# Kernel optimization log

Measured on AMD Instinct MI355X. Metric: run time of the kernel, lower is better.

Reference implementation:

```python
import jax, jax.numpy as jnp
import numpy as np

B, D, H, W = 64, 256, 32, 32
K, DC = 1024, 128  # codebook size, codebook dim = D // 2
BETA = 0.25


def setup_inputs() -> dict:
    key = jax.random.key(0)
    ks = jax.random.split(key, 4)
    return {
        "x": jax.random.normal(ks[0], (B, D, H, W), dtype=jnp.float32),
        "pre_W": jax.random.normal(ks[1], (DC, D), dtype=jnp.float32) * (1.0 / np.sqrt(D)),
        "pre_b": jnp.zeros((DC,), dtype=jnp.float32),
        "post_W": jax.random.normal(ks[2], (D, DC), dtype=jnp.float32) * (1.0 / np.sqrt(DC)),
        "post_b": jnp.zeros((D,), dtype=jnp.float32),
        "lookup_table": jax.random.normal(ks[3], (K, DC), dtype=jnp.float32) * (1.0 / np.sqrt(DC)),
    }


def reference(x, pre_W, pre_b, post_W, post_b, lookup_table):
    sg = jax.lax.stop_gradient
    b, d, h, w = x.shape
    # pre-quant 1x1 conv: [b, d, h, w] -> [b, dc, h, w]
    z = jnp.einsum("bchw,oc->bohw", x, pre_W) + pre_b[None, :, None, None]
    # flatten tokens: [b*h*w, dc]
    zf = z.transpose(0, 2, 3, 1).reshape(-1, DC)
    # squared distances to codebook (argmin identical to cdist argmin)
    d2 = (
        jnp.sum(zf * zf, axis=1, keepdims=True)
        - 2.0 * zf @ lookup_table.T
        + jnp.sum(lookup_table * lookup_table, axis=1)[None, :]
    )  # [N, K]
    q = jnp.argmin(d2, axis=1)  # [N]
    x_e = lookup_table[q].reshape(b, h, w, DC).transpose(0, 3, 1, 2)  # [b, dc, h, w]
    # losses (enable_ema_update = False path)
    codebook_loss = jnp.mean((sg(z) - x_e) ** 2)
    commitment_loss = BETA * jnp.mean((z - sg(x_e)) ** 2)
    loss = (1.0 - BETA) * codebook_loss + commitment_loss
    # straight-through estimator
    z_st = z + sg(x_e - z)
    # post-quant 1x1 conv: [b, dc, h, w] -> [b, d, h, w]
    out = jnp.einsum("bchw,oc->bohw", z_st, post_W) + post_b[None, :, None, None]
    # perplexity from empirical code usage
    counts = jnp.zeros((K,), dtype=jnp.float32).at[q].add(1.0)
    e_mean = counts / q.shape[0]
    perplexity = jnp.exp(-jnp.sum(e_mean * jnp.log(e_mean + 1e-10)))
    q_map = q.reshape(b, h, w)
    return out, loss, q_map, perplexity
```

## Files before the change

kernel.cpp:

```cpp
#include <hip/hip_runtime.h>
#include <cstdint>

#define NB   64
#define ND   256
#define NHW  1024
#define NTOK 65536
#define NDC  128
#define NK   1024

#define OFF_LOSS 16777216
#define OFF_Q    16777217
#define OFF_PERP 16842753

#define GAPTHR 1e-3f
#define NEGINF (-3.402823466e38f)

typedef short short8 __attribute__((ext_vector_type(8)));
typedef float f32x4 __attribute__((ext_vector_type(4)));

__device__ __forceinline__ unsigned short f2bf(float f) {
  unsigned u = __float_as_uint(f);
  u += 0x7FFFu + ((u >> 16) & 1u);
  return (unsigned short)(u >> 16);
}
__device__ __forceinline__ float bf2f(unsigned short h) {
  return __uint_as_float(((unsigned)h) << 16);
}

__device__ __forceinline__ void gll16(const void* g, void* l) {
  __builtin_amdgcn_global_load_lds(
      (const __attribute__((address_space(1))) unsigned int*)g,
      (__attribute__((address_space(3))) unsigned int*)l, 16, 0, 0);
}

__global__ __launch_bounds__(256) void k_init(
    const float* __restrict__ lut, const float* __restrict__ preW,
    const float* __restrict__ postW,
    unsigned short* __restrict__ ch,
    unsigned short* __restrict__ pwh, unsigned short* __restrict__ pwl,
    unsigned short* __restrict__ qwh, unsigned short* __restrict__ qwl,
    float* __restrict__ nhn, double* __restrict__ cn2d,
    int* __restrict__ counts, double* __restrict__ lossAcc, int* __restrict__ ctr) {
  int tid = blockIdx.x * 256 + threadIdx.x;
  int stride = gridDim.x * 256;
  for (int i = tid; i < NK * NDC; i += stride) {
    int code = i >> 7, c = i & 127;
    float f = lut[i];
    unsigned short h1 = f2bf(f);
    float r = f - bf2f(h1);
    ch[code * 256 + c] = h1;
    ch[code * 256 + 128 + c] = f2bf(r);
  }
  for (int i = tid; i < NDC * ND; i += stride) {
    float f = preW[i];
    unsigned u = __float_as_uint(f);
    float lf = f - __uint_as_float(u & 0xffff0000u);
    pwh[i] = (unsigned short)(u >> 16);
    pwl[i] = (unsigned short)(__float_as_uint(lf) >> 16);
  }
  for (int i = tid; i < ND * NDC; i += stride) {
    float f = postW[i];
    unsigned u = __float_as_uint(f);
    float lf = f - __uint_as_float(u & 0xffff0000u);
    qwh[i] = (unsigned short)(u >> 16);
    qwl[i] = (unsigned short)(__float_as_uint(lf) >> 16);
  }
  if (tid < NK) {
    float s = 0.f;
    double sd = 0.0;
    for (int c = 0; c < NDC; c++) {
      float v = lut[tid * NDC + c];
      s = fmaf(v, v, s);
      sd = fma((double)v, (double)v, sd);
    }
    nhn[tid] = -0.5f * s;
    cn2d[tid] = sd;
    counts[tid] = 0;
  }
  if (tid == 0) { *lossAcc = 0.0; *ctr = 0; }
}

__global__ __launch_bounds__(256, 1) void k_preconv(
    const float* __restrict__ x, const unsigned short* __restrict__ pwh,
    const unsigned short* __restrict__ pwl, const float* __restrict__ pre_b,
    float* __restrict__ zf) {
  __shared__ __align__(16) float xs[2][32 * 256];
  int bx = blockIdx.x;
  int b = bx >> 2, p0 = (bx & 3) * 256;
  int tid = threadIdx.x;
  int lane = tid & 63, w = tid >> 6;
  int g = lane >> 4, l15 = lane & 15;
  const char* xb = (const char*)(x + (size_t)b * (ND * NHW) + p0);

  #pragma unroll
  for (int i = 0; i < 8; ++i) {
    int o = i * 4096 + tid * 16;
    int chl = o >> 10;
    int col = (o & 1023) ^ (((chl >> 3) & 3) << 5);
    gll16(xb + (size_t)chl * 4096 + col, ((char*)&xs[0][0]) + o);
  }
  asm volatile("s_waitcnt vmcnt(0)" ::: "memory");
  __syncthreads();

  f32x4 acc[8][4];
  #pragma unroll
  for (int rt = 0; rt < 8; ++rt)
    #pragma unroll
    for (int ct = 0; ct < 4; ++ct) acc[rt][ct] = (f32x4){0.f, 0.f, 0.f, 0.f};

  int cur = 0;
  for (int ks = 0; ks < 8; ++ks) {
    if (ks < 7) {
      const char* gb = xb + (size_t)(ks + 1) * 32 * 4096;
      #pragma unroll
      for (int i = 0; i < 8; ++i) {
        int o = i * 4096 + tid * 16;
        int chl = o >> 10;
        int col = (o & 1023) ^ (((chl >> 3) & 3) << 5);
        gll16(gb + (size_t)chl * 4096 + col, ((char*)&xs[cur ^ 1][0]) + o);
      }
    }
    int k0 = ks * 32;
    short8 bh[4], bl[4];
    #pragma unroll
    for (int ct = 0; ct < 4; ++ct) {
      int tok = w * 64 + ct * 16 + l15;
      int tswz = tok ^ (g << 3);
      #pragma unroll
      for (int j = 0; j < 8; ++j) {
        float f = xs[cur][(g * 8 + j) * 256 + tswz];
        unsigned u = __float_as_uint(f);
        float lf = f - __uint_as_float(u & 0xffff0000u);
        bh[ct][j] = (short)(u >> 16);
        bl[ct][j] = (short)(__float_as_uint(lf) >> 16);
      }
    }
    #pragma unroll
    for (int rt = 0; rt < 8; ++rt) {
      short8 ah = *reinterpret_cast<const short8*>(&pwh[(rt * 16 + l15) * ND + k0 + g * 8]);
      short8 al = *reinterpret_cast<const short8*>(&pwl[(rt * 16 + l15) * ND + k0 + g * 8]);
      #pragma unroll
      for (int ct = 0; ct < 4; ++ct) {
        acc[rt][ct] = __builtin_amdgcn_mfma_f32_16x16x32_bf16(ah, bh[ct], acc[rt][ct], 0, 0, 0);
        acc[rt][ct] = __builtin_amdgcn_mfma_f32_16x16x32_bf16(ah, bl[ct], acc[rt][ct], 0, 0, 0);
        acc[rt][ct] = __builtin_amdgcn_mfma_f32_16x16x32_bf16(al, bh[ct], acc[rt][ct], 0, 0, 0);
      }
    }
    asm volatile("s_waitcnt vmcnt(0)" ::: "memory");
    __syncthreads();
    cur ^= 1;
  }

  #pragma unroll
  for (int rt = 0; rt < 8; ++rt) {
    float4 bb = *reinterpret_cast<const float4*>(&pre_b[rt * 16 + g * 4]);
    #pragma unroll
    for (int ct = 0; ct < 4; ++ct) {
      int n = bx * 256 + w * 64 + ct * 16 + l15;
      float4 v;
      v.x = acc[rt][ct][0] + bb.x;
      v.y = acc[rt][ct][1] + bb.y;
      v.z = acc[rt][ct][2] + bb.z;
      v.w = acc[rt][ct][3] + bb.w;
      *reinterpret_cast<float4*>(&zf[(size_t)n * NDC + rt * 16 + g * 4]) = v;
    }
  }
}

__global__ __launch_bounds__(256, 2) void k_dist(
    const float* __restrict__ zf, const unsigned short* __restrict__ ch,
    const float* __restrict__ nhn,
    int* __restrict__ q, int* __restrict__ list, int* __restrict__ ctr,
    double* __restrict__ lossAcc) {
  __shared__ __align__(16) short chbuf[2][8192];
  __shared__ float HnLds[NK];
  __shared__ float zn2Lds[4][2][16];
  __shared__ float red[256];
  int tid = threadIdx.x;
  int lane = tid & 63, w = tid >> 6;
  int g = lane >> 4;
  int n0 = blockIdx.x * 128;

  for (int i = tid; i < NK; i += 256) HnLds[i] = nhn[i];

  short8 az[2][8];
  {
    int arow = lane & 15;
    #pragma unroll
    for (int rt = 0; rt < 2; ++rt) {
      const float* zr = zf + (size_t)(n0 + w * 32 + rt * 16 + arow) * NDC;
      float sq = 0.f;
      #pragma unroll
      for (int f = 0; f < 4; ++f) {
        const float* p = zr + f * 32 + g * 8;
        float4 v0 = *reinterpret_cast<const float4*>(p);
        float4 v1 = *reinterpret_cast<const float4*>(p + 4);
        float vv[8] = {v0.x, v0.y, v0.z, v0.w, v1.x, v1.y, v1.z, v1.w};
        short8 hi, lo;
        #pragma unroll
        for (int j = 0; j < 8; ++j) {
          sq = fmaf(vv[j], vv[j], sq);
          unsigned short h1 = f2bf(vv[j]);
          float r = vv[j] - bf2f(h1);
          hi[j] = (short)h1;
          lo[j] = (short)f2bf(r);
        }
        az[rt][f] = hi;
        az[rt][4 + f] = lo;
      }
      sq += __shfl_xor(sq, 16, 64);
      sq += __shfl_xor(sq, 32, 64);
      if (g == 0) zn2Lds[w][rt][arow] = sq;
    }
  }

  float best[2][4], sec[2][4];
  int bidx[2][4];
  #pragma unroll
  for (int rt = 0; rt < 2; ++rt)
    #pragma unroll
    for (int r = 0; r < 4; ++r) { best[rt][r] = NEGINF; sec[rt][r] = NEGINF; bidx[rt][r] = 0; }

  const char* chg = (const char*)ch;
  {
    const char* gb = chg + 0;
    #pragma unroll
    for (int rr = 0; rr < 4; ++rr) {
      int o = rr * 4096 + tid * 16;
      int so = o ^ (((o >> 9) & 7) << 4);
      gll16(gb + so, ((char*)&chbuf[0][0]) + o);
    }
  }
  asm volatile("s_waitcnt vmcnt(0)" ::: "memory");
  __syncthreads();

  int cur = 0;
  for (int chunk = 0; chunk < 32; ++chunk) {
    if (chunk < 31) {
      const char* gb = chg + (chunk + 1) * 16384;
      #pragma unroll
      for (int rr = 0; rr < 4; ++rr) {
        int o = rr * 4096 + tid * 16;
        int so = o ^ (((o >> 9) & 7) << 4);
        gll16(gb + so, ((char*)&chbuf[cur ^ 1][0]) + o);
      }
    }
    const char* cb = (const char*)&chbuf[cur][0];
    for (int ct = 0; ct < 2; ++ct) {
      int codeg = chunk * 32 + ct * 16 + (lane & 15);
      float nh = HnLds[codeg];
      short8 bc[8];
      #pragma unroll
      for (int f = 0; f < 8; ++f) {
        int byte = ((lane & 15) + ct * 16) * 512 + f * 64 + g * 16;
        byte ^= ((lane & 7) << 4);
        bc[f] = *reinterpret_cast<const short8*>(cb + byte);
      }
      f32x4 acc0 = {nh, nh, nh, nh};
      f32x4 acc1 = {nh, nh, nh, nh};
      #pragma unroll
      for (int j = 0; j < 4; ++j) {
        acc0 = __builtin_amdgcn_mfma_f32_16x16x32_bf16(az[0][j], bc[j], acc0, 0, 0, 0);
        acc1 = __builtin_amdgcn_mfma_f32_16x16x32_bf16(az[1][j], bc[j], acc1, 0, 0, 0);
        acc0 = __builtin_amdgcn_mfma_f32_16x16x32_bf16(az[0][j], bc[4 + j], acc0, 0, 0, 0);
        acc1 = __builtin_amdgcn_mfma_f32_16x16x32_bf16(az[1][j], bc[4 + j], acc1, 0, 0, 0);
        acc0 = __builtin_amdgcn_mfma_f32_16x16x32_bf16(az[0][4 + j], bc[j], acc0, 0, 0, 0);
        acc1 = __builtin_amdgcn_mfma_f32_16x16x32_bf16(az[1][4 + j], bc[j], acc1, 0, 0, 0);
      }
      #pragma unroll
      for (int r = 0; r < 4; ++r) {
        float s0 = acc0[r];
        bool t0 = s0 > best[0][r];
        bidx[0][r] = t0 ? codeg : bidx[0][r];
        sec[0][r] = fmaxf(sec[0][r], fminf(s0, best[0][r]));
        best[0][r] = fmaxf(s0, best[0][r]);
        float s1 = acc1[r];
        bool t1 = s1 > best[1][r];
        bidx[1][r] = t1 ? codeg : bidx[1][r];
        sec[1][r] = fmaxf(sec[1][r], fminf(s1, best[1][r]));
        best[1][r] = fmaxf(s1, best[1][r]);
      }
    }
    asm volatile("s_waitcnt vmcnt(0)" ::: "memory");
    __syncthreads();
    cur ^= 1;
  }

  float lsum = 0.f;
  #pragma unroll
  for (int rt = 0; rt < 2; ++rt) {
    #pragma unroll
    for (int r = 0; r < 4; ++r) {
      float b = best[rt][r];
      float s2 = sec[rt][r];
      int bi_ = bidx[rt][r];
      #pragma unroll
      for (int m = 1; m < 16; m <<= 1) {
        float ob = __shfl_xor(b, m, 64);
        float os = __shfl_xor(s2, m, 64);
        int oi = __shfl_xor(bi_, m, 64);
        float ns = fmaxf(fmaxf(s2, os), fminf(b, ob));
        bool take = (ob > b) || (ob == b && oi < bi_);
        b = take ? ob : b;
        bi_ = take ? oi : bi_;
        s2 = ns;
      }
      if ((lane & 15) == 0) {
        int token = n0 + w * 32 + rt * 16 + g * 4 + r;
        q[token] = bi_;
        if (b - s2 < GAPTHR) {
          int pos = atomicAdd(ctr, 1);
          list[pos] = token;
        }
        lsum += zn2Lds[w][rt][g * 4 + r] - 2.0f * b;
      }
    }
  }
  red[tid] = lsum;
  __syncthreads();
  for (int s = 128; s > 0; s >>= 1) {
    if (tid < s) red[tid] += red[tid + s];
    __syncthreads();
  }
  if (tid == 0) atomicAdd(lossAcc, (double)red[0]);
}

__global__ __launch_bounds__(256) void k_rescore(
    const float* __restrict__ x, const float* __restrict__ preW,
    const float* __restrict__ pre_b, const float* __restrict__ lut,
    const double* __restrict__ cn2d,
    const int* __restrict__ list, const int* __restrict__ ctr, int* __restrict__ q) {
  __shared__ float xs[4][256];
  __shared__ double zs[4][128];
  __shared__ double rd[4][256];
  __shared__ int    rc[4][256];
  int nf = *ctr;
  int tid = threadIdx.x;
  int w = tid >> 6, lane = tid & 63;
  for (int g0 = blockIdx.x * 4; g0 < nf; g0 += gridDim.x * 4) {
    int nt = nf - g0; if (nt > 4) nt = 4;
    #pragma unroll
    for (int t = 0; t < 4; ++t) {
      int token = list[g0 + (t < nt ? t : 0)];
      int b = token >> 10, p = token & 1023;
      xs[t][tid] = x[(size_t)(b * ND + tid) * NHW + p];
    }
    __syncthreads();
    #pragma unroll
    for (int rep = 0; rep < 2; ++rep) {
      int idx = rep * 256 + tid;
      int t = idx >> 7, dc = idx & 127;
      double acc = (double)pre_b[dc];
      const float* wr = preW + (size_t)dc * ND;
      #pragma unroll 4
      for (int d = 0; d < ND; d += 4) {
        float4 wv = *reinterpret_cast<const float4*>(wr + d);
        acc = fma((double)wv.x, (double)xs[t][d + 0], acc);
        acc = fma((double)wv.y, (double)xs[t][d + 1], acc);
        acc = fma((double)wv.z, (double)xs[t][d + 2], acc);
        acc = fma((double)wv.w, (double)xs[t][d + 3], acc);
      }
      zs[t][dc] = acc;
    }
    __syncthreads();
    double bd[4]; int bc_[4];
    #pragma unroll
    for (int t = 0; t < 4; ++t) { bd[t] = 1e300; bc_[t] = 0x7fffffff; }
    for (int cc = 0; cc < 4; ++cc) {
      int c = cc * 256 + tid;
      const float* cr = lut + (size_t)c * NDC;
      double a0 = 0.0, a1 = 0.0, a2 = 0.0, a3 = 0.0;
      #pragma unroll 4
      for (int k = 0; k < NDC; ++k) {
        double lc = (double)cr[k];
        a0 = fma(zs[0][k], lc, a0);
        a1 = fma(zs[1][k], lc, a1);
        a2 = fma(zs[2][k], lc, a2);
        a3 = fma(zs[3][k], lc, a3);
      }
      double cn = cn2d[c];
      double d0 = cn - 2.0 * a0; if (d0 < bd[0]) { bd[0] = d0; bc_[0] = c; }
      double d1 = cn - 2.0 * a1; if (d1 < bd[1]) { bd[1] = d1; bc_[1] = c; }
      double d2 = cn - 2.0 * a2; if (d2 < bd[2]) { bd[2] = d2; bc_[2] = c; }
      double d3 = cn - 2.0 * a3; if (d3 < bd[3]) { bd[3] = d3; bc_[3] = c; }
    }
    #pragma unroll
    for (int t = 0; t < 4; ++t) { rd[t][tid] = bd[t]; rc[t][tid] = bc_[t]; }
    __syncthreads();
    {
      double b_ = rd[w][lane]; int c_ = rc[w][lane];
      #pragma unroll
      for (int s = 64; s < 256; s += 64) {
        double ob = rd[w][lane + s]; int oc = rc[w][lane + s];
        if (ob < b_ || (ob == b_ && oc < c_)) { b_ = ob; c_ = oc; }
      }
      #pragma unroll
      for (int m = 1; m < 64; m <<= 1) {
        double ob = __shfl_xor(b_, m, 64);
        int oc = __shfl_xor(c_, m, 64);
        if (ob < b_ || (ob == b_ && oc < c_)) { b_ = ob; c_ = oc; }
      }
      if (lane == 0 && w < nt) q[list[g0 + w]] = c_;
    }
    __syncthreads();
  }
}

__global__ __launch_bounds__(256, 3) void k_post(
    const float* __restrict__ lut,
    const int* __restrict__ q, const unsigned short* __restrict__ qwh,
    const unsigned short* __restrict__ qwl, const float* __restrict__ post_b,
    float* __restrict__ out,
    int* __restrict__ counts, float* __restrict__ outq) {
  int bx = blockIdx.x;
  int n0 = (bx >> 1) * 128;
  int oh = (bx & 1) * 128;
  int b = n0 >> 10, p0 = n0 & 1023;
  int tid = threadIdx.x;
  int lane = tid & 63, w = tid >> 6;
  int g = lane >> 4, l15 = lane & 15;

  int qv[2];
  #pragma unroll
  for (int ct = 0; ct < 2; ++ct) qv[ct] = q[n0 + w * 32 + ct * 16 + l15];

  float4 ga[2][4][2];
  #pragma unroll
  for (int ct = 0; ct < 2; ++ct) {
    const float* xr0 = lut + (size_t)qv[ct] * NDC + g * 8;
    #pragma unroll
    for (int ks = 0; ks < 4; ++ks) {
      ga[ct][ks][0] = *reinterpret_cast<const float4*>(xr0 + ks * 32);
      ga[ct][ks][1] = *reinterpret_cast<const float4*>(xr0 + ks * 32 + 4);
    }
  }

  if (tid < 64) {
    int n = n0 + ((bx & 1) << 6) + tid;
    int c = q[n];
    atomicAdd(&counts[c], 1);
    outq[n] = (float)c;
  }

  short8 ah[2][4], al[2][4];
  #pragma unroll
  for (int ct = 0; ct < 2; ++ct)
    #pragma unroll
    for (int ks = 0; ks < 4; ++ks) {
      float vv[8] = {ga[ct][ks][0].x, ga[ct][ks][0].y, ga[ct][ks][0].z, ga[ct][ks][0].w,
                     ga[ct][ks][1].x, ga[ct][ks][1].y, ga[ct][ks][1].z, ga[ct][ks][1].w};
      #pragma unroll
      for (int j = 0; j < 8; ++j) {
        unsigned u = __float_as_uint(vv[j]);
        float lf = vv[j] - __uint_as_float(u & 0xffff0000u);
        ah[ct][ks][j] = (short)(u >> 16);
        al[ct][ks][j] = (short)(__float_as_uint(lf) >> 16);
      }
    }

  f32x4 acc[8][2];
  #pragma unroll
  for (int nt = 0; nt < 8; ++nt)
    #pragma unroll
    for (int ct = 0; ct < 2; ++ct) acc[nt][ct] = (f32x4){0.f, 0.f, 0.f, 0.f};

  #pragma unroll
  for (int ks = 0; ks < 4; ++ks) {
    int k0 = ks * 32;
    #pragma unroll
    for (int nt = 0; nt < 8; ++nt) {
      short8 bh = *reinterpret_cast<const short8*>(&qwh[(size_t)(oh + nt * 16 + l15) * NDC + k0 + g * 8]);
      short8 bl = *reinterpret_cast<const short8*>(&qwl[(size_t)(oh + nt * 16 + l15) * NDC + k0 + g * 8]);
      #pragma unroll
      for (int ct = 0; ct < 2; ++ct) {
        acc[nt][ct] = __builtin_amdgcn_mfma_f32_16x16x32_bf16(ah[ct][ks], bh, acc[nt][ct], 0, 0, 0);
        acc[nt][ct] = __builtin_amdgcn_mfma_f32_16x16x32_bf16(al[ct][ks], bh, acc[nt][ct], 0, 0, 0);
        acc[nt][ct] = __builtin_amdgcn_mfma_f32_16x16x32_bf16(ah[ct][ks], bl, acc[nt][ct], 0, 0, 0);
      }
    }
  }
  #pragma unroll
  for (int nt = 0; nt < 8; ++nt) {
    int o = oh + nt * 16 + l15;
    float bias = post_b[o];
    float* orow = out + (size_t)(b * ND + o) * NHW;
    #pragma unroll
    for (int ct = 0; ct < 2; ++ct) {
      int p = p0 + w * 32 + ct * 16 + g * 4;
      float4 v;
      v.x = acc[nt][ct][0] + bias;
      v.y = acc[nt][ct][1] + bias;
      v.z = acc[nt][ct][2] + bias;
      v.w = acc[nt][ct][3] + bias;
      *reinterpret_cast<float4*>(orow + p) = v;
    }
  }
}

__global__ __launch_bounds__(256) void k_fin(
    const double* __restrict__ lossAcc, const int* __restrict__ counts,
    float* __restrict__ out_loss, float* __restrict__ out_perp) {
  __shared__ float red[256];
  int tid = threadIdx.x;
  float h = 0.f;
  for (int i = tid; i < NK; i += 256) {
    float e = (float)counts[i] * (1.0f / (float)NTOK);
    h += e * logf(e + 1e-10f);
  }
  red[tid] = h;
  __syncthreads();
  for (int s = 128; s > 0; s >>= 1) {
    if (tid < s) red[tid] += red[tid + s];
    __syncthreads();
  }
  if (tid == 0) {
    *out_perp = expf(-red[0]);
    *out_loss = (float)(*lossAcc / ((double)NTOK * (double)NDC));
  }
}

extern "C" void kernel_launch(void* const* d_in, const int* in_sizes, int n_in,
                              void* d_out, int out_size, void* d_ws, size_t ws_size,
                              hipStream_t stream) {
  const float* x     = (const float*)d_in[0];
  const float* preW  = (const float*)d_in[1];
  const float* preb  = (const float*)d_in[2];
  const float* postW = (const float*)d_in[3];
  const float* postb = (const float*)d_in[4];
  const float* lut   = (const float*)d_in[5];
  float* out = (float*)d_out;

  char* ws = (char*)d_ws;
  float*          zf      = (float*)(ws);
  unsigned short* ch      = (unsigned short*)(ws + 33554432);
  unsigned short* pwh     = (unsigned short*)(ws + 34078720);
  unsigned short* pwl     = (unsigned short*)(ws + 34144256);
  unsigned short* qwh     = (unsigned short*)(ws + 34209792);
  unsigned short* qwl     = (unsigned short*)(ws + 34275328);
  float*          nhn     = (float*)(ws + 34340864);
  int*            q       = (int*)  (ws + 34344960);
  int*            list    = (int*)  (ws + 34607104);
  int*            counts  = (int*)  (ws + 34869248);
  double*         lossAcc = (double*)(ws + 34873344);
  int*            ctr     = (int*)  (ws + 34873352);
  double*         cn2d    = (double*)(ws + 34873360);

  float* out_loss = out + OFF_LOSS;
  float* out_q    = out + OFF_Q;
  float* out_perp = out + OFF_PERP;

  hipLaunchKernelGGL(k_init, dim3(512), dim3(256), 0, stream,
                     lut, preW, postW, ch, pwh, pwl, qwh, qwl, nhn, cn2d,
                     counts, lossAcc, ctr);
  hipLaunchKernelGGL(k_preconv, dim3(256), dim3(256), 0, stream, x, pwh, pwl, preb, zf);
  hipLaunchKernelGGL(k_dist, dim3(512), dim3(256), 0, stream, zf, ch, nhn, q, list, ctr, lossAcc);
  hipLaunchKernelGGL(k_rescore, dim3(1024), dim3(256), 0, stream,
                     x, preW, preb, lut, cn2d, list, ctr, q);
  hipLaunchKernelGGL(k_post, dim3(1024), dim3(256), 0, stream,
                     lut, q, qwh, qwl, postb, out, counts, out_q);
  hipLaunchKernelGGL(k_fin, dim3(1), dim3(256), 0, stream, lossAcc, counts, out_loss, out_perp);
}
```

Before: 194.1 us.

## Split codebook across two half-blocks in k_dist and merge argmin in LDS

k_dist now runs 512 threads per block. Each half scans 512 of the 1024 codes for the same 128 tokens, so the serial chunk loop per wave is halved. The two partial best, second-best and index results are combined through shared memory before q, the near-tie list and the loss are written. This doubles the wave count and the shared codebook buffers per block. It also loads the z fragments redundantly in both halves and adds an extra barrier and merge step.

Result: slower. 207.7 us (+7.0%).

```diff
diff --git a/kernel.cpp b/kernel.cpp
--- a/kernel.cpp
+++ b/kernel.cpp
@@ -167,28 +167,33 @@
   }
 }
 
-__global__ __launch_bounds__(256, 2) void k_dist(
+__global__ __launch_bounds__(512, 2) void k_dist(
     const float* __restrict__ zf, const unsigned short* __restrict__ ch,
     const float* __restrict__ nhn,
     int* __restrict__ q, int* __restrict__ list, int* __restrict__ ctr,
     double* __restrict__ lossAcc) {
-  __shared__ __align__(16) short chbuf[2][8192];
+  __shared__ __align__(16) short chbuf[2][2][8192];
   __shared__ float HnLds[NK];
-  __shared__ float zn2Lds[4][2][16];
-  __shared__ float red[256];
+  __shared__ float zn2L[128];
+  __shared__ float bestL[2][128], secL[2][128];
+  __shared__ int   idxL[2][128];
+  __shared__ float red[512];
   int tid = threadIdx.x;
-  int lane = tid & 63, w = tid >> 6;
-  int g = lane >> 4;
+  int half = tid >> 8;
+  int t256 = tid & 255;
+  int lane = tid & 63;
+  int w4 = (tid >> 6) & 3;
+  int g = lane >> 4, l15 = lane & 15;
   int n0 = blockIdx.x * 128;
 
-  for (int i = tid; i < NK; i += 256) HnLds[i] = nhn[i];
+  for (int i = tid; i < NK; i += 512) HnLds[i] = nhn[i];
 
   short8 az[2][8];
   {
-    int arow = lane & 15;
+    int arow = l15;
     #pragma unroll
     for (int rt = 0; rt < 2; ++rt) {
-      const float* zr = zf + (size_t)(n0 + w * 32 + rt * 16 + arow) * NDC;
+      const float* zr = zf + (size_t)(n0 + w4 * 32 + rt * 16 + arow) * NDC;
       float sq = 0.f;
       #pragma unroll
       for (int f = 0; f < 4; ++f) {
@@ -210,7 +215,7 @@
       }
       sq += __shfl_xor(sq, 16, 64);
       sq += __shfl_xor(sq, 32, 64);
-      if (g == 0) zn2Lds[w][rt][arow] = sq;
+      if (half == 0 && g == 0) zn2L[w4 * 32 + rt * 16 + arow] = sq;
     }
   }
 
@@ -221,38 +226,37 @@
     #pragma unroll
     for (int r = 0; r < 4; ++r) { best[rt][r] = NEGINF; sec[rt][r] = NEGINF; bidx[rt][r] = 0; }
 
-  const char* chg = (const char*)ch;
+  const char* chg = (const char*)ch + (size_t)half * 262144;
   {
-    const char* gb = chg + 0;
     #pragma unroll
     for (int rr = 0; rr < 4; ++rr) {
-      int o = rr * 4096 + tid * 16;
+      int o = rr * 4096 + t256 * 16;
       int so = o ^ (((o >> 9) & 7) << 4);
-      gll16(gb + so, ((char*)&chbuf[0][0]) + o);
+      gll16(chg + so, ((char*)&chbuf[half][0][0]) + o);
     }
   }
   asm volatile("s_waitcnt vmcnt(0)" ::: "memory");
   __syncthreads();
 
   int cur = 0;
-  for (int chunk = 0; chunk < 32; ++chunk) {
-    if (chunk < 31) {
+  for (int chunk = 0; chunk < 16; ++chunk) {
+    if (chunk < 15) {
       const char* gb = chg + (chunk + 1) * 16384;
       #pragma unroll
       for (int rr = 0; rr < 4; ++rr) {
-        int o = rr * 4096 + tid * 16;
+        int o = rr * 4096 + t256 * 16;
         int so = o ^ (((o >> 9) & 7) << 4);
-        gll16(gb + so, ((char*)&chbuf[cur ^ 1][0]) + o);
-      }
-    }
-    const char* cb = (const char*)&chbuf[cur][0];
+        gll16(gb + so, ((char*)&chbuf[half][cur ^ 1][0]) + o);
+      }
+    }
+    const char* cb = (const char*)&chbuf[half][cur][0];
     for (int ct = 0; ct < 2; ++ct) {
-      int codeg = chunk * 32 + ct * 16 + (lane & 15);
+      int codeg = half * 512 + chunk * 32 + ct * 16 + l15;
       float nh = HnLds[codeg];
       short8 bc[8];
       #pragma unroll
       for (int f = 0; f < 8; ++f) {
-        int byte = ((lane & 15) + ct * 16) * 512 + f * 64 + g * 16;
+        int byte = (l15 + ct * 16) * 512 + f * 64 + g * 16;
         byte ^= ((lane & 7) << 4);
         bc[f] = *reinterpret_cast<const short8*>(cb + byte);
       }
@@ -286,7 +290,6 @@
     cur ^= 1;
   }
 
-  float lsum = 0.f;
   #pragma unroll
   for (int rt = 0; rt < 2; ++rt) {
     #pragma unroll
@@ -306,19 +309,36 @@
         s2 = ns;
       }
       if ((lane & 15) == 0) {
-        int token = n0 + w * 32 + rt * 16 + g * 4 + r;
-        q[token] = bi_;
-        if (b - s2 < GAPTHR) {
-          int pos = atomicAdd(ctr, 1);
-          list[pos] = token;
-        }
-        lsum += zn2Lds[w][rt][g * 4 + r] - 2.0f * b;
-      }
-    }
+        int tok = w4 * 32 + rt * 16 + g * 4 + r;
+        bestL[half][tok] = b;
+        secL[half][tok] = s2;
+        idxL[half][tok] = bi_;
+      }
+    }
+  }
+  __syncthreads();
+
+  float lsum = 0.f;
+  if (tid < 128) {
+    int t = tid;
+    float b1 = bestL[0][t], s1 = secL[0][t];
+    float b2 = bestL[1][t], s2 = secL[1][t];
+    int i1 = idxL[0][t], i2 = idxL[1][t];
+    bool take = b2 > b1;
+    float bb = take ? b2 : b1;
+    int ii = take ? i2 : i1;
+    float ss = fmaxf(fminf(b1, b2), take ? s2 : s1);
+    int token = n0 + t;
+    q[token] = ii;
+    if (bb - ss < GAPTHR) {
+      int pos = atomicAdd(ctr, 1);
+      list[pos] = token;
+    }
+    lsum = zn2L[t] - 2.0f * bb;
   }
   red[tid] = lsum;
   __syncthreads();
-  for (int s = 128; s > 0; s >>= 1) {
+  for (int s = 256; s > 0; s >>= 1) {
     if (tid < s) red[tid] += red[tid + s];
     __syncthreads();
   }
@@ -553,7 +573,7 @@
                      lut, preW, postW, ch, pwh, pwl, qwh, qwl, nhn, cn2d,
                      counts, lossAcc, ctr);
   hipLaunchKernelGGL(k_preconv, dim3(256), dim3(256), 0, stream, x, pwh, pwl, preb, zf);
-  hipLaunchKernelGGL(k_dist, dim3(512), dim3(256), 0, stream, zf, ch, nhn, q, list, ctr, lossAcc);
+  hipLaunchKernelGGL(k_dist, dim3(512), dim3(512), 0, stream, zf, ch, nhn, q, list, ctr, lossAcc);
   hipLaunchKernelGGL(k_rescore, dim3(1024), dim3(256), 0, stream,
                      x, preW, preb, lut, cn2d, list, ctr, q);
   hipLaunchKernelGGL(k_post, dim3(1024), dim3(256), 0, stream,
```
